# Kernel tuning notes

Measured on AMD Instinct MI355X. Metric: run time of the kernel, lower is better.

## Reference

```python
import jax, jax.numpy as jnp
import numpy as np

GROUP_SIZE = 32
FP8_MAX = 448.0
EPS = 1e-8


def fp8_pseudo_quantize_groupwise(x):
    """Per-group (contiguous groups of GROUP_SIZE along last dim) fp8-e4m3
    pseudo-quantization: scale to fp8 range, cast to fp8, cast back, rescale."""
    shape = x.shape
    g = shape[-1] // GROUP_SIZE
    xg = x.reshape(*shape[:-1], g, GROUP_SIZE)
    amax = jnp.max(jnp.abs(xg), axis=-1, keepdims=True)
    scale = jnp.maximum(amax, EPS) / FP8_MAX  # fp32 per-group scale
    q = (xg / scale).astype(jnp.float8_e4m3fn).astype(x.dtype)
    return (q * scale).reshape(shape)


def setup_inputs() -> dict:
    key = jax.random.key(0)
    k1, k2, k3 = jax.random.split(key, 3)
    B, S, K, N = 4, 2048, 4096, 4096
    x = jax.random.normal(k1, (B, S, K), dtype=jnp.float32)
    # Linear-like init scale for weight/bias
    W = jax.random.normal(k2, (N, K), dtype=jnp.float32) * (1.0 / np.sqrt(K))
    bias = jax.random.normal(k3, (N,), dtype=jnp.float32) * (1.0 / np.sqrt(K))
    return {"x": x, "W": W, "bias": bias}


def reference(x, W, bias):
    # pseudo mode, a_bit=8 < 16: quantize both activations and weight
    Wq = fp8_pseudo_quantize_groupwise(W)   # [N, K]
    xq = fp8_pseudo_quantize_groupwise(x)   # [B, S, K]
    # F.linear: xq @ Wq.T + bias
    out = jnp.einsum('bsk,nk->bsn', xq, Wq) + bias
    return out
```

## Files before the change

kernel.cpp:

```cpp
#include <hip/hip_runtime.h>
#include <hip/hip_bf16.h>

typedef __bf16 bf16x8 __attribute__((ext_vector_type(8)));
typedef float floatx4 __attribute__((ext_vector_type(4)));
typedef unsigned short ushortx8 __attribute__((ext_vector_type(8)));

#define FP8_MAX 448.0f
#define QEPS 1e-8f

#define GLLDS16(gptr, lptr)                                                          \
  __builtin_amdgcn_global_load_lds((const __attribute__((address_space(1))) void*)(gptr), \
                                   (__attribute__((address_space(3))) void*)(lptr), 16, 0, 0)

__global__ __launch_bounds__(256) void quant_dq_kernel(
    const float* __restrict__ src, __hip_bfloat16* __restrict__ dst, long long n)
{
    long long t = (long long)blockIdx.x * blockDim.x + threadIdx.x;
    long long base = t * 8;
    if (base >= n) return;

    const float4 v0 = *(const float4*)(src + base);
    const float4 v1 = *(const float4*)(src + base + 4);

    float am = fmaxf(
        fmaxf(fmaxf(fabsf(v0.x), fabsf(v0.y)), fmaxf(fabsf(v0.z), fabsf(v0.w))),
        fmaxf(fmaxf(fabsf(v1.x), fabsf(v1.y)), fmaxf(fabsf(v1.z), fabsf(v1.w))));
    am = fmaxf(am, __shfl_xor(am, 1));
    am = fmaxf(am, __shfl_xor(am, 2));
    const float scale = fmaxf(am, QEPS) / FP8_MAX;

    int p0 = __builtin_amdgcn_cvt_pk_fp8_f32(v0.x / scale, v0.y / scale, 0, false);
    int p1 = __builtin_amdgcn_cvt_pk_fp8_f32(v0.z / scale, v0.w / scale, 0, false);
    int p2 = __builtin_amdgcn_cvt_pk_fp8_f32(v1.x / scale, v1.y / scale, 0, false);
    int p3 = __builtin_amdgcn_cvt_pk_fp8_f32(v1.z / scale, v1.w / scale, 0, false);

    float r0 = __builtin_amdgcn_cvt_f32_fp8(p0, 0) * scale;
    float r1 = __builtin_amdgcn_cvt_f32_fp8(p0, 1) * scale;
    float r2 = __builtin_amdgcn_cvt_f32_fp8(p1, 0) * scale;
    float r3 = __builtin_amdgcn_cvt_f32_fp8(p1, 1) * scale;
    float r4 = __builtin_amdgcn_cvt_f32_fp8(p2, 0) * scale;
    float r5 = __builtin_amdgcn_cvt_f32_fp8(p2, 1) * scale;
    float r6 = __builtin_amdgcn_cvt_f32_fp8(p3, 0) * scale;
    float r7 = __builtin_amdgcn_cvt_f32_fp8(p3, 1) * scale;

    alignas(16) __hip_bfloat16 hb[8] = {
        __float2bfloat16(r0), __float2bfloat16(r1),
        __float2bfloat16(r2), __float2bfloat16(r3),
        __float2bfloat16(r4), __float2bfloat16(r5),
        __float2bfloat16(r6), __float2bfloat16(r7)};
    *(ushortx8*)(dst + base) = *(const ushortx8*)hb;
}

__global__ __launch_bounds__(256, 2) void gemm_bias_kernel(
    const __hip_bfloat16* __restrict__ A,
    const __hip_bfloat16* __restrict__ B,
    const float* __restrict__ bias,
    float* __restrict__ C,
    int M, int N, int K)
{
    __shared__ __attribute__((aligned(16))) __hip_bfloat16 As[128 * 64];
    __shared__ __attribute__((aligned(16))) __hip_bfloat16 Bs[128 * 64];

    const int tid  = threadIdx.x;
    const int lane = tid & 63;
    const int wave = tid >> 6;
    const int wr   = (wave >> 1) * 64;
    const int wc   = (wave & 1) * 64;

    const long bm = (long)blockIdx.y * 128;
    const long bn = (long)blockIdx.x * 128;

    const int srow = tid >> 3;
    const int scg  = (tid & 7) ^ (srow & 7);

    const __hip_bfloat16* gA = A + (bm + srow) * (long)K + scg * 8;
    const __hip_bfloat16* gB = B + (bn + srow) * (long)K + scg * 8;
    const long rstep = 32 * (long)K;

    __hip_bfloat16* lA = As + tid * 8;
    __hip_bfloat16* lB = Bs + tid * 8;

    floatx4 acc[4][4];
#pragma unroll
    for (int i = 0; i < 4; ++i)
#pragma unroll
        for (int j = 0; j < 4; ++j)
            acc[i][j] = (floatx4){0.f, 0.f, 0.f, 0.f};

    const int fr = lane & 15;
    const int fq = lane >> 4;

    for (int k0 = 0; k0 < K; k0 += 64) {
#pragma unroll
        for (int r = 0; r < 4; ++r) {
            GLLDS16(gA + k0 + r * rstep, lA + r * 32 * 64);
            GLLDS16(gB + k0 + r * rstep, lB + r * 32 * 64);
        }
        __syncthreads();

#pragma unroll
        for (int ks = 0; ks < 2; ++ks) {
            bf16x8 af[4], bfv[4];
#pragma unroll
            for (int i = 0; i < 4; ++i) {
                const int ra = wr + i * 16 + fr;
                af[i] = *(const bf16x8*)(As + ra * 64 + (((ks * 4 + fq) ^ (ra & 7)) * 8));
            }
#pragma unroll
            for (int j = 0; j < 4; ++j) {
                const int rb = wc + j * 16 + fr;
                bfv[j] = *(const bf16x8*)(Bs + rb * 64 + (((ks * 4 + fq) ^ (rb & 7)) * 8));
            }
#pragma unroll
            for (int i = 0; i < 4; ++i)
#pragma unroll
                for (int j = 0; j < 4; ++j)
                    acc[i][j] = __builtin_amdgcn_mfma_f32_16x16x32_bf16(af[i], bfv[j], acc[i][j], 0, 0, 0);
        }
        __syncthreads();
    }

    const int rq = (lane >> 4) * 4;
#pragma unroll
    for (int j = 0; j < 4; ++j) {
        const long gc = bn + wc + j * 16 + fr;
        const float bj = bias[gc];
#pragma unroll
        for (int i = 0; i < 4; ++i) {
            const long gr = bm + wr + i * 16 + rq;
            float* cp = C + gr * (long)N + gc;
#pragma unroll
            for (int r = 0; r < 4; ++r)
                cp[(long)r * N] = acc[i][j][r] + bj;
        }
    }
}

extern "C" void kernel_launch(void* const* d_in, const int* in_sizes, int n_in,
                              void* d_out, int out_size, void* d_ws, size_t ws_size,
                              hipStream_t stream) {
    const float* x    = (const float*)d_in[0];
    const float* W    = (const float*)d_in[1];
    const float* bias = (const float*)d_in[2];
    float* out = (float*)d_out;

    const long long nx = in_sizes[0];
    const long long nw = in_sizes[1];
    const int N = in_sizes[2];
    const int K = (int)(nw / N);
    const int M = (int)(nx / K);

    __hip_bfloat16* xq = (__hip_bfloat16*)d_ws;
    __hip_bfloat16* wq = xq + nx;

    {
        long long tx = nx / 8;
        int blocks = (int)((tx + 255) / 256);
        quant_dq_kernel<<<blocks, 256, 0, stream>>>(x, xq, nx);
    }
    {
        long long tw = nw / 8;
        int blocks = (int)((tw + 255) / 256);
        quant_dq_kernel<<<blocks, 256, 0, stream>>>(W, wq, nw);
    }

    dim3 grid(N / 128, M / 128);
    gemm_bias_kernel<<<grid, 256, 0, stream>>>(xq, wq, bias, out, M, N, K);
}
```

Before: 510.1 us.

## Rewrite GEMM as 256x256 double-buffered, 8-wave pipelined kernel with grid swizzle

The bf16 GEMM moves from a 128x128 tile with 4 waves and a single LDS buffer to a 256x256 tile with 8 waves and double-buffered LDS. Global-to-LDS loads for upcoming k-tiles are interleaved with MFMA quadrants under explicit vmcnt/lgkmcnt waits, barriers and setprio. A 1D grid with an XCD-style block swizzle is added. This targets load latency stalls and low arithmetic intensity per tile, at the cost of 128 KB of LDS per block and heavy register pressure, which may limit occupancy.

```diff
diff --git a/kernel.cpp b/kernel.cpp
--- a/kernel.cpp
+++ b/kernel.cpp
@@ -51,87 +51,179 @@
     *(ushortx8*)(dst + base) = *(const ushortx8*)hb;
 }
 
-__global__ __launch_bounds__(256, 2) void gemm_bias_kernel(
+
+#define BAR() __builtin_amdgcn_s_barrier()
+#define LGKM0()                                              \
+  do {                                                       \
+    asm volatile("s_waitcnt lgkmcnt(0)" ::: "memory");       \
+    __builtin_amdgcn_sched_barrier(0);                       \
+  } while (0)
+#define VMCNT(n) asm volatile("s_waitcnt vmcnt(" #n ")" ::: "memory")
+
+#define STAGE_A(a_, t_, b_)                                                   \
+  do {                                                                        \
+    const __hip_bfloat16* g_ = gAs + (long)(a_) * 128 * K + (long)(t_) * 64;  \
+    __hip_bfloat16* l_ = &sA[(b_)][(a_) * 8192 + tid * 8];                    \
+    GLLDS16(g_, l_);                                                          \
+    GLLDS16(g_ + 64 * (long)K, l_ + 4096);                                    \
+  } while (0)
+
+#define STAGE_B(a_, t_, b_)                                                   \
+  do {                                                                        \
+    const __hip_bfloat16* g_ = gBs + (long)(a_) * 128 * K + (long)(t_) * 64;  \
+    __hip_bfloat16* l_ = &sB[(b_)][(a_) * 8192 + tid * 8];                    \
+    GLLDS16(g_, l_);                                                          \
+    GLLDS16(g_ + 64 * (long)K, l_ + 4096);                                    \
+  } while (0)
+
+#define LOAD_A(buf, mh)                                                       \
+  do {                                                                        \
+    _Pragma("unroll") for (int mm = 0; mm < 4; ++mm)                          \
+    _Pragma("unroll") for (int ks = 0; ks < 2; ++ks)                          \
+        af[mm][ks] = *(const bf16x8*)((buf) + ((mh)*4 + mm) * 1024 + aoff[ks]); \
+  } while (0)
+
+#define LOAD_B(buf, nh)                                                       \
+  do {                                                                        \
+    _Pragma("unroll") for (int nn = 0; nn < 2; ++nn)                          \
+    _Pragma("unroll") for (int ks = 0; ks < 2; ++ks)                          \
+        bfr[nh][nn][ks] = *(const bf16x8*)((buf) + (nh)*2048 + nn * 1024 + boff[ks]); \
+  } while (0)
+
+#define QUAD(mh, nh)                                                          \
+  do {                                                                        \
+    __builtin_amdgcn_s_setprio(1);                                            \
+    _Pragma("unroll") for (int ks = 0; ks < 2; ++ks)                          \
+    _Pragma("unroll") for (int mm = 0; mm < 4; ++mm)                          \
+    _Pragma("unroll") for (int nn = 0; nn < 2; ++nn)                          \
+        acc[(mh)*4 + mm][(nh)*2 + nn] = __builtin_amdgcn_mfma_f32_16x16x32_bf16( \
+            af[mm][ks], bfr[nh][nn][ks], acc[(mh)*4 + mm][(nh)*2 + nn], 0, 0, 0); \
+    __builtin_amdgcn_s_setprio(0);                                            \
+  } while (0)
+
+__global__ __launch_bounds__(512, 2) void gemm_bias_kernel(
     const __hip_bfloat16* __restrict__ A,
     const __hip_bfloat16* __restrict__ B,
     const float* __restrict__ bias,
     float* __restrict__ C,
     int M, int N, int K)
 {
-    __shared__ __attribute__((aligned(16))) __hip_bfloat16 As[128 * 64];
-    __shared__ __attribute__((aligned(16))) __hip_bfloat16 Bs[128 * 64];
+    __shared__ __attribute__((aligned(16))) __hip_bfloat16 sA[2][256 * 64];
+    __shared__ __attribute__((aligned(16))) __hip_bfloat16 sB[2][256 * 64];
 
     const int tid  = threadIdx.x;
     const int lane = tid & 63;
     const int wave = tid >> 6;
-    const int wr   = (wave >> 1) * 64;
-    const int wc   = (wave & 1) * 64;
-
-    const long bm = (long)blockIdx.y * 128;
-    const long bn = (long)blockIdx.x * 128;
-
-    const int srow = tid >> 3;
-    const int scg  = (tid & 7) ^ (srow & 7);
-
-    const __hip_bfloat16* gA = A + (bm + srow) * (long)K + scg * 8;
-    const __hip_bfloat16* gB = B + (bn + srow) * (long)K + scg * 8;
-    const long rstep = 32 * (long)K;
-
-    __hip_bfloat16* lA = As + tid * 8;
-    __hip_bfloat16* lB = Bs + tid * 8;
-
-    floatx4 acc[4][4];
-#pragma unroll
-    for (int i = 0; i < 4; ++i)
+    const int wm   = wave >> 2;
+    const int wn   = wave & 3;
+
+    const int nwg = gridDim.x;
+    const int wg  = blockIdx.x;
+    int swz = wg;
+    if ((nwg & 7) == 0) swz = (wg & 7) * (nwg >> 3) + (wg >> 3);
+    const int NXB = N >> 8;
+    const long bm = (long)(swz / NXB) * 256;
+    const long bn = (long)(swz % NXB) * 256;
+
+    const int srow   = tid >> 3;
+    const int schunk = (tid & 7) ^ (srow & 7);
+    const __hip_bfloat16* gAs = A + (bm + srow) * (long)K + schunk * 8;
+    const __hip_bfloat16* gBs = B + (bn + srow) * (long)K + schunk * 8;
+
+    const int fr = lane & 15;
+    const int fq = lane >> 4;
+    const int f7 = fr & 7;
+    int aoff[2], boff[2];
+#pragma unroll
+    for (int ks = 0; ks < 2; ++ks) {
+        const int ch = ((ks * 4 + fq) ^ f7) * 8;
+        aoff[ks] = (wm * 128 + fr) * 64 + ch;
+        boff[ks] = (wn * 64 + fr) * 64 + ch;
+    }
+
+    floatx4 acc[8][4];
+#pragma unroll
+    for (int i = 0; i < 8; ++i)
 #pragma unroll
         for (int j = 0; j < 4; ++j)
             acc[i][j] = (floatx4){0.f, 0.f, 0.f, 0.f};
 
-    const int fr = lane & 15;
-    const int fq = lane >> 4;
-
-    for (int k0 = 0; k0 < K; k0 += 64) {
-#pragma unroll
-        for (int r = 0; r < 4; ++r) {
-            GLLDS16(gA + k0 + r * rstep, lA + r * 32 * 64);
-            GLLDS16(gB + k0 + r * rstep, lB + r * 32 * 64);
-        }
-        __syncthreads();
-
-#pragma unroll
-        for (int ks = 0; ks < 2; ++ks) {
-            bf16x8 af[4], bfv[4];
-#pragma unroll
-            for (int i = 0; i < 4; ++i) {
-                const int ra = wr + i * 16 + fr;
-                af[i] = *(const bf16x8*)(As + ra * 64 + (((ks * 4 + fq) ^ (ra & 7)) * 8));
-            }
-#pragma unroll
-            for (int j = 0; j < 4; ++j) {
-                const int rb = wc + j * 16 + fr;
-                bfv[j] = *(const bf16x8*)(Bs + rb * 64 + (((ks * 4 + fq) ^ (rb & 7)) * 8));
-            }
-#pragma unroll
-            for (int i = 0; i < 4; ++i)
-#pragma unroll
-                for (int j = 0; j < 4; ++j)
-                    acc[i][j] = __builtin_amdgcn_mfma_f32_16x16x32_bf16(af[i], bfv[j], acc[i][j], 0, 0, 0);
-        }
-        __syncthreads();
+    bf16x8 af[4][2];
+    bf16x8 bfr[2][2][2];
+
+    const int NT = K >> 6;
+    const int NI = NT >> 1;
+
+    STAGE_A(0, 0, 0); STAGE_A(1, 0, 0);
+    STAGE_B(0, 0, 0); STAGE_B(1, 0, 0);
+    if (NT > 1) { STAGE_B(0, 1, 1); STAGE_B(1, 1, 1); STAGE_A(0, 1, 1); }
+    VMCNT(6);
+    BAR();
+
+#pragma unroll 1
+    for (int i = 0; i < NI; ++i) {
+        const bool more = (i + 1 < NI);
+        const int t1 = 2 * i + 1, t2 = 2 * i + 2, t3 = 2 * i + 3;
+
+        LOAD_A(sA[0], 0); LOAD_B(sB[0], 0);
+        STAGE_A(1, t1, 1);
+        BAR(); LGKM0();
+        QUAD(0, 0);
+        BAR();
+
+        LOAD_B(sB[0], 1);
+        BAR(); LGKM0();
+        QUAD(0, 1);
+        BAR();
+
+        LOAD_A(sA[0], 1);
+        if (more) STAGE_B(0, t2, 0);
+        BAR(); LGKM0();
+        QUAD(1, 0);
+        BAR();
+
+        if (more) { STAGE_B(1, t2, 0); STAGE_A(0, t2, 0); }
+        BAR();
+        QUAD(1, 1);
+        if (more) { VMCNT(6); } else { VMCNT(0); }
+        BAR();
+
+        LOAD_A(sA[1], 0); LOAD_B(sB[1], 0);
+        if (more) STAGE_A(1, t2, 0);
+        BAR(); LGKM0();
+        QUAD(0, 0);
+        BAR();
+
+        LOAD_B(sB[1], 1);
+        BAR(); LGKM0();
+        QUAD(0, 1);
+        BAR();
+
+        LOAD_A(sA[1], 1);
+        if (more) STAGE_B(0, t3, 1);
+        BAR(); LGKM0();
+        QUAD(1, 0);
+        BAR();
+
+        if (more) { STAGE_B(1, t3, 1); STAGE_A(0, t3, 1); }
+        BAR();
+        QUAD(1, 1);
+        if (more) { VMCNT(6); }
+        BAR();
     }
 
     const int rq = (lane >> 4) * 4;
 #pragma unroll
     for (int j = 0; j < 4; ++j) {
-        const long gc = bn + wc + j * 16 + fr;
+        const long gc = bn + wn * 64 + j * 16 + fr;
         const float bj = bias[gc];
 #pragma unroll
-        for (int i = 0; i < 4; ++i) {
-            const long gr = bm + wr + i * 16 + rq;
+        for (int mf = 0; mf < 8; ++mf) {
+            const long gr = bm + wm * 128 + mf * 16 + rq;
             float* cp = C + gr * (long)N + gc;
 #pragma unroll
             for (int r = 0; r < 4; ++r)
-                cp[(long)r * N] = acc[i][j][r] + bj;
+                cp[(long)r * N] = acc[mf][j][r] + bj;
         }
     }
 }
@@ -164,6 +256,6 @@
         quant_dq_kernel<<<blocks, 256, 0, stream>>>(W, wq, nw);
     }
 
-    dim3 grid(N / 128, M / 128);
-    gemm_bias_kernel<<<grid, 256, 0, stream>>>(xq, wq, bias, out, M, N, K);
+    dim3 grid((N / 256) * (M / 256));
+    gemm_bias_kernel<<<grid, 512, 0, stream>>>(xq, wq, bias, out, M, N, K);
 }
```

After: 532.2 us. 4.3% more time.
